# Kernel tuning notes

Hardware: AMD Instinct MI355X
Metric: run time of the kernel (lower is better)

Reference implementation:

```python
import jax, jax.numpy as jnp
import numpy as np

B, T = 192, 50
VOCAB = 24000
EMBED = 300
HID2 = 2000          # 2*HIDDEN_SIZE
MAXOUT = 300         # DIMEN_MAXOUT_UNIT
QV = 300             # DIMEN_QUALITY_VECTOR
H2 = 100             # LSTM hidden


def setup_inputs():
    key = jax.random.key(0)
    ks = jax.random.split(key, 24)
    s = 0.02
    inp = {
        'dec_out': jax.random.normal(ks[0], (B, T, HID2), jnp.float32),
        'y': jax.random.randint(ks[1], (B, T), 0, VOCAB, jnp.int64 if jax.config.jax_enable_x64 else jnp.int32),
        'contex': jax.random.normal(ks[2], (B, T, HID2), jnp.float32),
        'embed_table': jax.random.normal(ks[3], (VOCAB, EMBED), jnp.float32) * s,
        'W1': jax.random.uniform(ks[4], (VOCAB, QV), jnp.float32),  # torch.rand
        'S_w': jax.random.normal(ks[5], (2 * MAXOUT, HID2), jnp.float32) * s,
        'S_b': jnp.zeros((2 * MAXOUT,), jnp.float32),
        'V_w': jax.random.normal(ks[6], (2 * MAXOUT, 2 * EMBED), jnp.float32) * s,
        'V_b': jnp.zeros((2 * MAXOUT,), jnp.float32),
        'C0_w': jax.random.normal(ks[7], (2 * MAXOUT, HID2), jnp.float32) * s,
        'C0_b': jnp.zeros((2 * MAXOUT,), jnp.float32),
        'W2_w': jax.random.normal(ks[8], (QV, MAXOUT), jnp.float32) * s,
        'W2_b': jnp.zeros((QV,), jnp.float32),
        'wih0': jax.random.normal(ks[9], (4 * H2, QV), jnp.float32) * s,
        'whh0': jax.random.normal(ks[10], (4 * H2, H2), jnp.float32) * s,
        'bih0': jnp.zeros((4 * H2,), jnp.float32),
        'bhh0': jnp.zeros((4 * H2,), jnp.float32),
        'wih1': jax.random.normal(ks[11], (4 * H2, H2), jnp.float32) * s,
        'whh1': jax.random.normal(ks[12], (4 * H2, H2), jnp.float32) * s,
        'bih1': jnp.zeros((4 * H2,), jnp.float32),
        'bhh1': jnp.zeros((4 * H2,), jnp.float32),
        'Wqe_w': jax.random.normal(ks[13], (1, H2), jnp.float32) * s,
        'Wqe_b': jnp.zeros((1,), jnp.float32),
    }
    return inp


def _lstm_layer(x, Wih, Whh, bih, bhh):
    # x: [B, T, D] -> outputs [B, T, H]; torch gate order i, f, g, o
    Bb = x.shape[0]
    H = Whh.shape[1]
    xT = jnp.swapaxes(x, 0, 1)  # [T, B, D]

    def step(carry, xt):
        h, c = carry
        g = xt @ Wih.T + h @ Whh.T + bih + bhh
        i, f, gg, o = jnp.split(g, 4, axis=-1)
        i = jax.nn.sigmoid(i); f = jax.nn.sigmoid(f)
        gg = jnp.tanh(gg); o = jax.nn.sigmoid(o)
        c = f * c + i * gg
        h = o * jnp.tanh(c)
        return (h, c), h

    h0 = jnp.zeros((Bb, H), x.dtype)
    (_, _), hs = jax.lax.scan(step, (h0, h0), xT)
    return jnp.swapaxes(hs, 0, 1)


def reference(dec_out, y, contex, embed_table, W1, S_w, S_b, V_w, V_b,
              C0_w, C0_b, W2_w, W2_b, wih0, whh0, bih0, bhh0,
              wih1, whh1, bih1, bhh1, Wqe_w, Wqe_b):
    Bb, Tt, _ = dec_out.shape
    embed = embed_table[y]  # [B, T, EMBED]
    idx = jnp.arange(Tt)
    li = jnp.where(idx == 0, 1, idx - 1)          # left neighbor (i==0 -> 1)
    ri = jnp.where(idx == Tt - 1, Tt - 2, idx + 1)  # right neighbor (i==T-1 -> T-2)
    tensor2 = jnp.concatenate([embed[:, li], embed[:, ri]], axis=-1)  # [B,T,600]
    t_long = (dec_out @ S_w.T + S_b) + (tensor2 @ V_w.T + V_b) + (contex @ C0_w.T + C0_b)
    # maxout over consecutive pairs: t[...,i] = max(t_long[...,2i], t_long[...,2i+1])
    t = t_long.reshape(Bb, Tt, MAXOUT, 2).max(axis=-1)
    a = t @ W2_w.T + W2_b                        # [B,T,QV]
    logits = a @ W1.T                            # [B,T,VOCAB]
    b = jax.nn.log_softmax(logits.reshape(Bb * Tt, -1), axis=1)
    quality = W1[y] * a                          # [B,T,QV]
    mask = (y == 0)
    index1 = jnp.where(mask.any(axis=1), mask.argmax(axis=1), Tt - 1)
    h = _lstm_layer(quality, wih0, whh0, bih0, bhh0)
    h = _lstm_layer(h, wih1, whh1, bih1, bhh1)   # [B,T,H2]
    s_sel = h[jnp.arange(Bb), index1]            # [B,H2]
    QE_score = jax.nn.sigmoid(s_sel @ Wqe_w.T + Wqe_b)  # [B,1]
    return (b, QE_score)
```

## Files before the change

kernel.cpp:

```cpp
#include <hip/hip_runtime.h>

typedef unsigned short u16;
typedef __attribute__((ext_vector_type(4))) float f32x4;
typedef __attribute__((ext_vector_type(8))) short bf16x8;
typedef __attribute__((ext_vector_type(4))) unsigned short u16x4;
typedef __attribute__((ext_vector_type(8))) unsigned short u16x8;

#define BT 9600
#define VOCAB 24000
#define NCB 188

__device__ __forceinline__ u16 f2b(float f){
  union { float f; unsigned u; } c; c.f = f;
  unsigned u = c.u;
  return (u16)((u + 0x7FFFu + ((u >> 16) & 1u)) >> 16);
}
__device__ __forceinline__ float b2f(u16 v){
  union { unsigned u; float f; } c; c.u = ((unsigned)v) << 16;
  return c.f;
}

#define GLD16(g, l) __builtin_amdgcn_global_load_lds( \
    (__attribute__((address_space(1))) void*)(g), \
    (__attribute__((address_space(3))) void*)(l), 16, 0, 0)

__device__ __forceinline__ void gemm_core(
    const u16* __restrict__ A, const u16* __restrict__ B,
    int K, int brow, int bcol, u16* As, u16* Bs, f32x4 acc[4][4])
{
  const int tid  = threadIdx.x;
  const int w    = tid >> 6;
  const int lane = tid & 63;
  const int wm = w >> 1, wn = w & 1;

  const f32x4 fz = {0.f, 0.f, 0.f, 0.f};
  #pragma unroll
  for (int m = 0; m < 4; ++m)
    #pragma unroll
    for (int n = 0; n < 4; ++n) acc[m][n] = fz;

  const int nkt = K >> 6;

  auto stage = [&](int kt, int buf) {
    #pragma unroll
    for (int i = 0; i < 4; ++i) {
      int gl  = i * 256 + tid;
      int row = gl >> 3;
      int g   = (gl & 7) ^ (row & 7);
      const u16* ga = A + (size_t)(brow + row) * K + (kt << 6) + (g << 3);
      GLD16(ga, As + buf * 8192 + (size_t)(i * 256 + w * 64) * 8);
      const u16* gb = B + (size_t)(bcol + row) * K + (kt << 6) + (g << 3);
      GLD16(gb, Bs + buf * 8192 + (size_t)(i * 256 + w * 64) * 8);
    }
  };

  stage(0, 0);
  int cur = 0;
  for (int kt = 0; kt < nkt; ++kt) {
    if (kt + 1 < nkt) {
      stage(kt + 1, cur ^ 1);
      asm volatile("s_waitcnt vmcnt(8)" ::: "memory");
    } else {
      asm volatile("s_waitcnt vmcnt(0)" ::: "memory");
    }
    __builtin_amdgcn_s_barrier();
    asm volatile("" ::: "memory");
    const u16* Ab = As + cur * 8192;
    const u16* Bb = Bs + cur * 8192;
    #pragma unroll
    for (int kk = 0; kk < 2; ++kk) {
      bf16x8 af[4], bf[4];
      #pragma unroll
      for (int m = 0; m < 4; ++m) {
        int row = wm * 64 + m * 16 + (lane & 15);
        int g   = (kk * 4 + (lane >> 4)) ^ (row & 7);
        af[m] = *(const bf16x8*)(Ab + row * 64 + g * 8);
      }
      #pragma unroll
      for (int n = 0; n < 4; ++n) {
        int row = wn * 64 + n * 16 + (lane & 15);
        int g   = (kk * 4 + (lane >> 4)) ^ (row & 7);
        bf[n] = *(const bf16x8*)(Bb + row * 64 + g * 8);
      }
      #pragma unroll
      for (int m = 0; m < 4; ++m)
        #pragma unroll
        for (int n = 0; n < 4; ++n)
          acc[m][n] = __builtin_amdgcn_mfma_f32_16x16x32_bf16(af[m], bf[n], acc[m][n], 0, 0, 0);
    }
    asm volatile("" ::: "memory");
    __builtin_amdgcn_s_barrier();
    cur ^= 1;
  }
}

__device__ __forceinline__ void prep_main_body(
    const float* __restrict__ dec, const float* __restrict__ ctx,
    u16* __restrict__ Xcat, int tid)
{
  if (tid >= 9600 * 500) return;
  int r = tid / 500, k8 = (tid % 500) * 8;
  const float* src = (k8 < 2000) ? dec + (size_t)r * 2000 + k8
                                 : ctx + (size_t)r * 2000 + (k8 - 2000);
  const float4* s4 = (const float4*)src;
  float4 v0 = s4[0], v1 = s4[1];
  u16x8 o;
  o[0] = f2b(v0.x); o[1] = f2b(v0.y); o[2] = f2b(v0.z); o[3] = f2b(v0.w);
  o[4] = f2b(v1.x); o[5] = f2b(v1.y); o[6] = f2b(v1.z); o[7] = f2b(v1.w);
  *(u16x8*)(Xcat + (size_t)r * 4608 + k8) = o;
}

__device__ __forceinline__ void prep_emb_body(
    const int* __restrict__ y, const float* __restrict__ etab,
    u16* __restrict__ Xcat, int tid)
{
  if (tid >= 9600 * 152) return;
  int r = tid / 152, u = tid % 152;
  u16* xr = Xcat + (size_t)r * 4608;
  if (u >= 150) {
    int base = (u == 150) ? 4300 : 4604;
    u16x4 z; z[0] = 0; z[1] = 0; z[2] = 0; z[3] = 0;
    *(u16x4*)(xr + base) = z;
    return;
  }
  int t = r % 50;
  int side = u / 75, j4 = (u % 75) * 4;
  int tt = (side == 0) ? (t == 0 ? 1 : t - 1) : (t == 49 ? 48 : t + 1);
  int tok = y[r - t + tt];
  float4 v = *(const float4*)(etab + (size_t)tok * 300 + j4);
  u16x4 o; o[0] = f2b(v.x); o[1] = f2b(v.y); o[2] = f2b(v.z); o[3] = f2b(v.w);
  *(u16x4*)(xr + (side == 0 ? 4000 : 4304) + j4) = o;
}

__device__ __forceinline__ void wcat_body(
    const float* __restrict__ Sw, const float* __restrict__ C0w, const float* __restrict__ Vw,
    const float* __restrict__ Sb, const float* __restrict__ Vb, const float* __restrict__ C0b,
    u16* __restrict__ Wcat, float* __restrict__ biasc, int tid)
{
  if (tid >= 640 * 4608) return;
  int n = tid / 4608, k = tid % 4608;
  float v = 0.f;
  if (n < 600) {
    if (k < 2000)                  v = Sw[n * 2000 + k];
    else if (k < 4000)             v = C0w[n * 2000 + (k - 2000)];
    else if (k < 4300)             v = Vw[n * 600 + (k - 4000)];
    else if (k >= 4304 && k < 4604) v = Vw[n * 600 + 300 + (k - 4304)];
  }
  Wcat[tid] = f2b(v);
  if (k == 0) biasc[n] = (n < 600) ? (Sb[n] + Vb[n] + C0b[n]) : 0.f;
}

__device__ __forceinline__ void conv_body(
    const float* __restrict__ src, u16* __restrict__ dst,
    int srows, int scols, int drows, int dcols4, int tid)
{
  if (tid >= drows * dcols4) return;
  int r = tid / dcols4, c4 = (tid % dcols4) * 4;
  u16x4 o; o[0] = 0; o[1] = 0; o[2] = 0; o[3] = 0;
  if (r < srows && c4 < scols) {
    float4 v = *(const float4*)(src + (size_t)r * scols + c4);
    o[0] = f2b(v.x); o[1] = f2b(v.y); o[2] = f2b(v.z); o[3] = f2b(v.w);
  }
  *(u16x4*)(dst + (size_t)r * (dcols4 * 4) + c4) = o;
}

__global__ __launch_bounds__(256) void k_prep_all(
    const float* __restrict__ dec, const float* __restrict__ ctx,
    const int* __restrict__ y, const float* __restrict__ etab,
    const float* __restrict__ Sw, const float* __restrict__ C0w,
    const float* __restrict__ Vw, const float* __restrict__ Sb,
    const float* __restrict__ Vb, const float* __restrict__ C0b,
    const float* __restrict__ W1, const float* __restrict__ W2w,
    const float* __restrict__ wih0, const float* __restrict__ wih1,
    u16* __restrict__ Xcat, u16* __restrict__ Wcat, float* __restrict__ biasc,
    u16* __restrict__ W1b, u16* __restrict__ W2b,
    u16* __restrict__ wih0b, u16* __restrict__ wih1b)
{
  int bid = blockIdx.x, th = threadIdx.x;
  if (bid < 18750)      prep_main_body(dec, ctx, Xcat, bid * 256 + th);
  else if (bid < 24450) prep_emb_body(y, etab, Xcat, (bid - 18750) * 256 + th);
  else if (bid < 35970) wcat_body(Sw, C0w, Vw, Sb, Vb, C0b, Wcat, biasc, (bid - 24450) * 256 + th);
  else if (bid < 43490) conv_body(W1,   W1b,   24000, 300, 24064, 80, (bid - 35970) * 256 + th);
  else if (bid < 43610) conv_body(W2w,  W2b,   300,   300, 384,   80, (bid - 43490) * 256 + th);
  else if (bid < 43770) conv_body(wih0, wih0b, 400,   300, 512,   80, (bid - 43610) * 256 + th);
  else                  conv_body(wih1, wih1b, 400,   100, 512,   32, (bid - 43770) * 256 + th);
}

__global__ __launch_bounds__(256) void k_gemm_tlong(
    const u16* __restrict__ Xcat, const u16* __restrict__ Wcat,
    const float* __restrict__ biasc, u16* __restrict__ tb)
{
  __shared__ u16 As[16384], Bs[16384];
  f32x4 acc[4][4];
  int brow = blockIdx.y * 128, bcol = blockIdx.x * 128;
  gemm_core(Xcat, Wcat, 4608, brow, bcol, As, Bs, acc);
  int lane = threadIdx.x & 63, w = threadIdx.x >> 6;
  int wm = w >> 1, wn = w & 1;
  #pragma unroll
  for (int m = 0; m < 4; ++m)
    #pragma unroll
    for (int n = 0; n < 4; ++n)
      #pragma unroll
      for (int r = 0; r < 4; ++r) {
        int row = brow + wm * 64 + m * 16 + ((lane >> 4) << 2) + r;
        int col = bcol + wn * 64 + n * 16 + (lane & 15);
        float v = acc[m][n][r] + biasc[col];
        float o = __shfl_xor(v, 1);
        float t = fmaxf(v, o);
        if ((lane & 1) == 0)
          tb[(size_t)row * 320 + (col >> 1)] = f2b(t);
      }
}

__global__ __launch_bounds__(256) void k_gemm_a(
    const u16* __restrict__ tb, const u16* __restrict__ W2b,
    const float* __restrict__ W2bias, const float* __restrict__ W1,
    const int* __restrict__ y, u16* __restrict__ ab, u16* __restrict__ qb)
{
  __shared__ u16 As[16384], Bs[16384];
  f32x4 acc[4][4];
  int brow = blockIdx.y * 128, bcol = blockIdx.x * 128;
  gemm_core(tb, W2b, 320, brow, bcol, As, Bs, acc);
  int lane = threadIdx.x & 63, w = threadIdx.x >> 6;
  int wm = w >> 1, wn = w & 1;
  #pragma unroll
  for (int m = 0; m < 4; ++m)
    #pragma unroll
    for (int n = 0; n < 4; ++n)
      #pragma unroll
      for (int r = 0; r < 4; ++r) {
        int row = brow + wm * 64 + m * 16 + ((lane >> 4) << 2) + r;
        int col = bcol + wn * 64 + n * 16 + (lane & 15);
        if (col < 320) {
          float bias = (col < 300) ? W2bias[col] : 0.f;
          float a = acc[m][n][r] + bias;
          ab[(size_t)row * 320 + col] = f2b(a);
          float q = 0.f;
          if (col < 300) {
            int yv = y[row];
            q = a * W1[(size_t)yv * 300 + col];
          }
          qb[(size_t)row * 320 + col] = f2b(q);
        }
      }
}

__global__ __launch_bounds__(256) void k_gemm_logits_bf16(
    const u16* __restrict__ ab, const u16* __restrict__ W1b,
    u16* __restrict__ lb, float* __restrict__ part, int rb0)
{
  __shared__ u16 smem[32768];
  __shared__ float rowsum[128][2];
  f32x4 acc[4][4];
  int brow = (rb0 + blockIdx.y) * 128, bcol = blockIdx.x * 128;
  gemm_core(ab, W1b, 320, brow, bcol, smem, smem + 16384, acc);
  int lane = threadIdx.x & 63, w = threadIdx.x >> 6;
  int wm = w >> 1, wn = w & 1;
  #pragma unroll
  for (int m = 0; m < 4; ++m)
    #pragma unroll
    for (int r = 0; r < 4; ++r) {
      int lrow = wm * 64 + m * 16 + ((lane >> 4) << 2) + r;
      float es = 0.f;
      #pragma unroll
      for (int n = 0; n < 4; ++n) {
        int lcol = wn * 64 + n * 16 + (lane & 15);
        float v = acc[m][n][r];
        smem[lrow * 136 + lcol] = f2b(v);
        if (bcol + lcol < VOCAB) es += __expf(v);
      }
      es += __shfl_xor(es, 1); es += __shfl_xor(es, 2);
      es += __shfl_xor(es, 4); es += __shfl_xor(es, 8);
      if ((lane & 15) == 0) rowsum[lrow][wn] = es;
    }
  __syncthreads();
  if (threadIdx.x < 128)
    part[(size_t)(brow + threadIdx.x) * NCB + blockIdx.x] =
        rowsum[threadIdx.x][0] + rowsum[threadIdx.x][1];
  int lrow_base = blockIdx.y * 128;
  #pragma unroll
  for (int j = 0; j < 8; ++j) {
    int ch   = j * 256 + threadIdx.x;
    int rowl = ch >> 4;
    int c16  = (ch & 15) << 3;
    u16x8 v = *(const u16x8*)(smem + rowl * 136 + c16);
    *(u16x8*)(lb + (size_t)(lrow_base + rowl) * 24064 + bcol + c16) = v;
  }
}

__global__ __launch_bounds__(256) void k_gemm_logits_f32(
    const u16* __restrict__ ab, const u16* __restrict__ W1b,
    float* __restrict__ dout, float* __restrict__ part)
{
  __shared__ u16 As[16384], Bs[16384];
  __shared__ float rowsum[128][2];
  f32x4 acc[4][4];
  int brow = blockIdx.y * 128, bcol = blockIdx.x * 128;
  gemm_core(ab, W1b, 320, brow, bcol, As, Bs, acc);
  int lane = threadIdx.x & 63, w = threadIdx.x >> 6;
  int wm = w >> 1, wn = w & 1;
  #pragma unroll
  for (int m = 0; m < 4; ++m)
    #pragma unroll
    for (int r = 0; r < 4; ++r) {
      int lrow = wm * 64 + m * 16 + ((lane >> 4) << 2) + r;
      size_t grow = (size_t)(brow + lrow);
      float es = 0.f;
      #pragma unroll
      for (int n = 0; n < 4; ++n) {
        int col = bcol + wn * 64 + n * 16 + (lane & 15);
        float v = acc[m][n][r];
        if (col < VOCAB) {
          dout[grow * VOCAB + col] = v;
          es += __expf(v);
        }
      }
      es += __shfl_xor(es, 1); es += __shfl_xor(es, 2);
      es += __shfl_xor(es, 4); es += __shfl_xor(es, 8);
      if ((lane & 15) == 0) rowsum[lrow][wn] = es;
    }
  __syncthreads();
  if (threadIdx.x < 128)
    part[(size_t)(brow + threadIdx.x) * NCB + blockIdx.x] =
        rowsum[threadIdx.x][0] + rowsum[threadIdx.x][1];
}

__global__ __launch_bounds__(256) void k_gemm_proj(
    const u16* __restrict__ Ab, const u16* __restrict__ Bb, int K,
    const float* __restrict__ b1, const float* __restrict__ b2, float* __restrict__ out)
{
  __shared__ u16 As[16384], Bs[16384];
  f32x4 acc[4][4];
  int brow = blockIdx.y * 128, bcol = blockIdx.x * 128;
  gemm_core(Ab, Bb, K, brow, bcol, As, Bs, acc);
  int lane = threadIdx.x & 63, w = threadIdx.x >> 6;
  int wm = w >> 1, wn = w & 1;
  #pragma unroll
  for (int m = 0; m < 4; ++m)
    #pragma unroll
    for (int n = 0; n < 4; ++n)
      #pragma unroll
      for (int r = 0; r < 4; ++r) {
        int row = brow + wm * 64 + m * 16 + ((lane >> 4) << 2) + r;
        int col = bcol + wn * 64 + n * 16 + (lane & 15);
        if (col < 400)
          out[(size_t)row * 400 + col] = acc[m][n][r] + b1[col] + b2[col];
      }
}

__global__ __launch_bounds__(256) void k_rowlog(
    const float* __restrict__ part, float* __restrict__ logl, int r0)
{
  int row = r0 + blockIdx.x * 4 + (threadIdx.x >> 6);
  int l = threadIdx.x & 63;
  const float* p = part + (size_t)row * NCB;
  float s = p[l] + p[l + 64] + (l < 60 ? p[l + 128] : 0.f);
  s += __shfl_xor(s, 1);  s += __shfl_xor(s, 2);  s += __shfl_xor(s, 4);
  s += __shfl_xor(s, 8);  s += __shfl_xor(s, 16); s += __shfl_xor(s, 32);
  if (l == 0) logl[row] = logf(s);
}

__global__ __launch_bounds__(256) void k_fixup(
    float4* __restrict__ out4, const float* __restrict__ logl)
{
  size_t i = (size_t)blockIdx.x * blockDim.x + threadIdx.x;
  size_t stride = (size_t)gridDim.x * blockDim.x;
  const size_t total = (size_t)BT * (VOCAB / 4);
  for (; i < total; i += stride) {
    size_t row = i / (VOCAB / 4);
    float l = logl[row];
    float4 v = out4[i];
    v.x -= l; v.y -= l; v.z -= l; v.w -= l;
    out4[i] = v;
  }
}

__global__ __launch_bounds__(256) void k_fixup_bf16(
    const u16* __restrict__ lb, const float* __restrict__ logl,
    float* __restrict__ out, int r0, int nrows)
{
  size_t i = (size_t)blockIdx.x * blockDim.x + threadIdx.x;
  size_t stride = (size_t)gridDim.x * blockDim.x;
  const size_t total = (size_t)nrows * (VOCAB / 8);
  for (; i < total; i += stride) {
    size_t rowl = i / (VOCAB / 8);
    int c8 = (int)(i % (VOCAB / 8)) * 8;
    size_t row = r0 + rowl;
    float l = logl[row];
    u16x8 v = *(const u16x8*)(lb + rowl * 24064 + c8);
    float4 o0, o1;
    o0.x = b2f(v[0]) - l; o0.y = b2f(v[1]) - l; o0.z = b2f(v[2]) - l; o0.w = b2f(v[3]) - l;
    o1.x = b2f(v[4]) - l; o1.y = b2f(v[5]) - l; o1.z = b2f(v[6]) - l; o1.w = b2f(v[7]) - l;
    float* op = out + row * VOCAB + c8;
    *(float4*)op = o0;
    *(float4*)(op + 4) = o1;
  }
}

__global__ __launch_bounds__(512) void k_lstm0(
    const float* __restrict__ xp0, const float* __restrict__ whh0, u16* __restrict__ h0b)
{
  int b = blockIdx.x, g = threadIdx.x;
  __shared__ float h[100];
  __shared__ float act[400];
  float wrow[100];
  if (g < 400) {
    const float4* wr = (const float4*)(whh0 + (size_t)g * 100);
    #pragma unroll
    for (int q = 0; q < 25; ++q) {
      float4 t = wr[q];
      wrow[4 * q] = t.x; wrow[4 * q + 1] = t.y; wrow[4 * q + 2] = t.z; wrow[4 * q + 3] = t.w;
    }
  }
  if (g < 100) h[g] = 0.f;
  float c = 0.f;
  __syncthreads();
  for (int t = 0; t < 50; ++t) {
    if (g < 400) {
      float s = xp0[(size_t)(b * 50 + t) * 400 + g];
      const float4* hv = (const float4*)h;
      #pragma unroll
      for (int q = 0; q < 25; ++q) {
        float4 hh = hv[q];
        s += wrow[4 * q] * hh.x + wrow[4 * q + 1] * hh.y
           + wrow[4 * q + 2] * hh.z + wrow[4 * q + 3] * hh.w;
      }
      act[g] = (g >= 200 && g < 300) ? tanhf(s) : 1.f / (1.f + __expf(-s));
    }
    __syncthreads();
    if (g < 100) {
      c = act[100 + g] * c + act[g] * act[200 + g];
      float hn = act[300 + g] * tanhf(c);
      h[g] = hn;
      h0b[(size_t)(b * 50 + t) * 128 + g] = f2b(hn);
    } else if (g < 128) {
      h0b[(size_t)(b * 50 + t) * 128 + g] = 0;
    }
    __syncthreads();
  }
}

__global__ __launch_bounds__(512) void k_lstm1(
    const float* __restrict__ xp1, const float* __restrict__ whh1,
    const int* __restrict__ y, const float* __restrict__ wqe,
    const float* __restrict__ wqeb, float* __restrict__ qout)
{
  int b = blockIdx.x, g = threadIdx.x;
  __shared__ float h[100];
  __shared__ float act[400];
  __shared__ float hsel[100];
  __shared__ int idx1;
  float wrow[100];
  if (g < 400) {
    const float4* wr = (const float4*)(whh1 + (size_t)g * 100);
    #pragma unroll
    for (int q = 0; q < 25; ++q) {
      float4 t = wr[q];
      wrow[4 * q] = t.x; wrow[4 * q + 1] = t.y; wrow[4 * q + 2] = t.z; wrow[4 * q + 3] = t.w;
    }
  }
  if (g == 0) {
    int ix = 49;
    for (int t = 0; t < 50; ++t) { if (y[b * 50 + t] == 0) { ix = t; break; } }
    idx1 = ix;
  }
  if (g < 100) { h[g] = 0.f; hsel[g] = 0.f; }
  float c = 0.f;
  __syncthreads();
  for (int t = 0; t < 50; ++t) {
    if (g < 400) {
      float s = xp1[(size_t)(b * 50 + t) * 400 + g];
      const float4* hv = (const float4*)h;
      #pragma unroll
      for (int q = 0; q < 25; ++q) {
        float4 hh = hv[q];
        s += wrow[4 * q] * hh.x + wrow[4 * q + 1] * hh.y
           + wrow[4 * q + 2] * hh.z + wrow[4 * q + 3] * hh.w;
      }
      act[g] = (g >= 200 && g < 300) ? tanhf(s) : 1.f / (1.f + __expf(-s));
    }
    __syncthreads();
    if (g < 100) {
      c = act[100 + g] * c + act[g] * act[200 + g];
      float hn = act[300 + g] * tanhf(c);
      h[g] = hn;
      if (t == idx1) hsel[g] = hn;
    }
    __syncthreads();
  }
  if (g == 0) {
    float s = wqeb[0];
    for (int j = 0; j < 100; ++j) s += hsel[j] * wqe[j];
    qout[b] = 1.f / (1.f + __expf(-s));
  }
}

extern "C" void kernel_launch(void* const* d_in, const int* in_sizes, int n_in,
                              void* d_out, int out_size, void* d_ws, size_t ws_size,
                              hipStream_t stream) {
  const float* dec  = (const float*)d_in[0];
  const int*   y    = (const int*)d_in[1];
  const float* ctx  = (const float*)d_in[2];
  const float* etab = (const float*)d_in[3];
  const float* W1   = (const float*)d_in[4];
  const float* Sw   = (const float*)d_in[5];
  const float* Sb   = (const float*)d_in[6];
  const float* Vw   = (const float*)d_in[7];
  const float* Vb   = (const float*)d_in[8];
  const float* C0w  = (const float*)d_in[9];
  const float* C0b  = (const float*)d_in[10];
  const float* W2w  = (const float*)d_in[11];
  const float* W2bias = (const float*)d_in[12];
  const float* wih0 = (const float*)d_in[13];
  const float* whh0 = (const float*)d_in[14];
  const float* bih0 = (const float*)d_in[15];
  const float* bhh0 = (const float*)d_in[16];
  const float* wih1 = (const float*)d_in[17];
  const float* whh1 = (const float*)d_in[18];
  const float* bih1 = (const float*)d_in[19];
  const float* bhh1 = (const float*)d_in[20];
  const float* wqe  = (const float*)d_in[21];
  const float* wqeb = (const float*)d_in[22];

  char* ws = (char*)d_ws;
  u16*   Xcat  = (u16*)(ws + 0);
  u16*   Wcat  = (u16*)(ws + 88473600);
  float* biasc = (float*)(ws + 94371840);
  u16*   tb    = (u16*)(ws + 94374400);
  u16*   W2b   = (u16*)(ws + 100518400);
  u16*   ab    = (u16*)(ws + 100764160);
  u16*   qb    = (u16*)(ws + 106908160);
  u16*   W1b   = (u16*)(ws + 113052160);
  float* part  = (float*)(ws + 128453120);
  float* logl  = (float*)(ws + 135672320);
  u16*   wih0b = (u16*)(ws + 135710720);
  float* xp0   = (float*)(ws + 136038400);
  u16*   h0b   = (u16*)(ws + 151398400);
  u16*   wih1b = (u16*)(ws + 153856000);
  float* xp1   = (float*)(ws + 153987072);
  u16*   lb    = (u16*)(ws + 169347072);
  const size_t WS_NEED_BF16 = 169347072ull + 154009600ull;
  const bool use_bf16_logits = (ws_size >= WS_NEED_BF16);

  float* bout  = (float*)d_out;
  float* qeout = bout + (size_t)BT * VOCAB;

  k_prep_all<<<43834, 256, 0, stream>>>(dec, ctx, y, etab, Sw, C0w, Vw, Sb, Vb, C0b,
                                        W1, W2w, wih0, wih1,
                                        Xcat, Wcat, biasc, W1b, W2b, wih0b, wih1b);

  k_gemm_tlong<<<dim3(5, 75), 256, 0, stream>>>(Xcat, Wcat, biasc, tb);
  k_gemm_a<<<dim3(3, 75), 256, 0, stream>>>(tb, W2b, W2bias, W1, y, ab, qb);

  if (use_bf16_logits) {
    for (int c = 0; c < 3; ++c) {
      k_gemm_logits_bf16<<<dim3(NCB, 25), 256, 0, stream>>>(ab, W1b, lb, part, 25 * c);
      k_rowlog<<<800, 256, 0, stream>>>(part, logl, 3200 * c);
      k_fixup_bf16<<<2048, 256, 0, stream>>>(lb, logl, bout, 3200 * c, 3200);
    }
  } else {
    k_gemm_logits_f32<<<dim3(NCB, 75), 256, 0, stream>>>(ab, W1b, bout, part);
    k_rowlog<<<2400, 256, 0, stream>>>(part, logl, 0);
    k_fixup<<<4096, 256, 0, stream>>>((float4*)bout, logl);
  }

  k_gemm_proj<<<dim3(4, 75), 256, 0, stream>>>(qb, wih0b, 320, bih0, bhh0, xp0);
  k_lstm0<<<192, 512, 0, stream>>>(xp0, whh0, h0b);
  k_gemm_proj<<<dim3(4, 75), 256, 0, stream>>>(h0b, wih1b, 128, bih1, bhh1, xp1);
  k_lstm1<<<192, 512, 0, stream>>>(xp1, whh1, y, wqe, wqeb, qeout);
}
```

Before: 1.048 ms.

## Fuse serial LSTM chain into logits/softmax stages via heterogeneous block launches

Replaces the three-chunk logits/rowlog/fixup loop and the separate LSTM kernels with four combined kernels. Each combined kernel assigns some blocks to the bandwidth-heavy logits, rowlog or fixup work and others to the latency-bound LSTM steps and projections, so the serial LSTM chain overlaps with them. It also remaps the t_long GEMM block indices so neighbouring row tiles land on the same XCD. The bf16 logits buffer now has to hold all 9600 rows, so the workspace requirement grows. If the workspace is too small, the code falls back to the f32 path and gets no overlap.

```diff
diff --git a/kernel.cpp b/kernel.cpp
--- a/kernel.cpp
+++ b/kernel.cpp
@@ -28,7 +28,7 @@
     const u16* __restrict__ A, const u16* __restrict__ B,
     int K, int brow, int bcol, u16* As, u16* Bs, f32x4 acc[4][4])
 {
-  const int tid  = threadIdx.x;
+  const int tid  = threadIdx.x & 255;
   const int w    = tid >> 6;
   const int lane = tid & 63;
   const int wm = w >> 1, wn = w & 1;
@@ -92,6 +92,27 @@
     __builtin_amdgcn_s_barrier();
     cur ^= 1;
   }
+}
+
+__device__ __forceinline__ void proj_epilogue(
+    f32x4 acc[4][4], int brow, int bcol,
+    const float* __restrict__ b1, const float* __restrict__ b2,
+    float* __restrict__ out)
+{
+  int tid = threadIdx.x & 255;
+  int lane = tid & 63, w = tid >> 6;
+  int wm = w >> 1, wn = w & 1;
+  #pragma unroll
+  for (int m = 0; m < 4; ++m)
+    #pragma unroll
+    for (int n = 0; n < 4; ++n)
+      #pragma unroll
+      for (int r = 0; r < 4; ++r) {
+        int row = brow + wm * 64 + m * 16 + ((lane >> 4) << 2) + r;
+        int col = bcol + wn * 64 + n * 16 + (lane & 15);
+        if (col < 400)
+          out[(size_t)row * 400 + col] = acc[m][n][r] + b1[col] + b2[col];
+      }
 }
 
 __device__ __forceinline__ void prep_main_body(
@@ -192,7 +213,12 @@
 {
   __shared__ u16 As[16384], Bs[16384];
   f32x4 acc[4][4];
-  int brow = blockIdx.y * 128, bcol = blockIdx.x * 128;
+  int L = blockIdx.x;
+  int xcd = L & 7, s = L >> 3;
+  int yy = (s / 5) * 8 + xcd;
+  int xx = s % 5;
+  if (yy >= 75) return;
+  int brow = yy * 128, bcol = xx * 128;
   gemm_core(Xcat, Wcat, 4608, brow, bcol, As, Bs, acc);
   int lane = threadIdx.x & 63, w = threadIdx.x >> 6;
   int wm = w >> 1, wn = w & 1;
@@ -245,14 +271,25 @@
       }
 }
 
-__global__ __launch_bounds__(256) void k_gemm_logits_bf16(
+__global__ __launch_bounds__(256) void k_s1(
     const u16* __restrict__ ab, const u16* __restrict__ W1b,
-    u16* __restrict__ lb, float* __restrict__ part, int rb0)
+    u16* __restrict__ lb, float* __restrict__ part,
+    const u16* __restrict__ qb, const u16* __restrict__ wih0b,
+    const float* __restrict__ bih0, const float* __restrict__ bhh0,
+    float* __restrict__ xp0)
 {
   __shared__ u16 smem[32768];
   __shared__ float rowsum[128][2];
   f32x4 acc[4][4];
-  int brow = (rb0 + blockIdx.y) * 128, bcol = blockIdx.x * 128;
+  int bid = blockIdx.x;
+  if (bid < 300) {
+    int brow = (bid / 4) * 128, bcol = (bid % 4) * 128;
+    gemm_core(qb, wih0b, 320, brow, bcol, smem, smem + 16384, acc);
+    proj_epilogue(acc, brow, bcol, bih0, bhh0, xp0);
+    return;
+  }
+  int g = bid - 300;
+  int brow = (g / NCB) * 128, bcol = (g % NCB) * 128;
   gemm_core(ab, W1b, 320, brow, bcol, smem, smem + 16384, acc);
   int lane = threadIdx.x & 63, w = threadIdx.x >> 6;
   int wm = w >> 1, wn = w & 1;
@@ -275,17 +312,191 @@
     }
   __syncthreads();
   if (threadIdx.x < 128)
-    part[(size_t)(brow + threadIdx.x) * NCB + blockIdx.x] =
+    part[(size_t)(brow + threadIdx.x) * NCB + (g % NCB)] =
         rowsum[threadIdx.x][0] + rowsum[threadIdx.x][1];
-  int lrow_base = blockIdx.y * 128;
   #pragma unroll
   for (int j = 0; j < 8; ++j) {
     int ch   = j * 256 + threadIdx.x;
     int rowl = ch >> 4;
     int c16  = (ch & 15) << 3;
     u16x8 v = *(const u16x8*)(smem + rowl * 136 + c16);
-    *(u16x8*)(lb + (size_t)(lrow_base + rowl) * 24064 + bcol + c16) = v;
-  }
+    *(u16x8*)(lb + (size_t)(brow + rowl) * 24064 + bcol + c16) = v;
+  }
+}
+
+__device__ __forceinline__ void lstm0_body(
+    const float* __restrict__ xp0, const float* __restrict__ whh0,
+    u16* __restrict__ h0b, int b)
+{
+  int g = threadIdx.x;
+  __shared__ float h[100];
+  __shared__ float act[400];
+  float wrow[100];
+  if (g < 400) {
+    const float4* wr = (const float4*)(whh0 + (size_t)g * 100);
+    #pragma unroll
+    for (int q = 0; q < 25; ++q) {
+      float4 t = wr[q];
+      wrow[4 * q] = t.x; wrow[4 * q + 1] = t.y; wrow[4 * q + 2] = t.z; wrow[4 * q + 3] = t.w;
+    }
+  }
+  if (g < 100) h[g] = 0.f;
+  float c = 0.f;
+  __syncthreads();
+  for (int t = 0; t < 50; ++t) {
+    if (g < 400) {
+      float s = xp0[(size_t)(b * 50 + t) * 400 + g];
+      const float4* hv = (const float4*)h;
+      #pragma unroll
+      for (int q = 0; q < 25; ++q) {
+        float4 hh = hv[q];
+        s += wrow[4 * q] * hh.x + wrow[4 * q + 1] * hh.y
+           + wrow[4 * q + 2] * hh.z + wrow[4 * q + 3] * hh.w;
+      }
+      act[g] = (g >= 200 && g < 300) ? tanhf(s) : 1.f / (1.f + __expf(-s));
+    }
+    __syncthreads();
+    if (g < 100) {
+      c = act[100 + g] * c + act[g] * act[200 + g];
+      float hn = act[300 + g] * tanhf(c);
+      h[g] = hn;
+      h0b[(size_t)(b * 50 + t) * 128 + g] = f2b(hn);
+    } else if (g < 128) {
+      h0b[(size_t)(b * 50 + t) * 128 + g] = 0;
+    }
+    __syncthreads();
+  }
+}
+
+__device__ __forceinline__ void lstm1_body(
+    const float* __restrict__ xp1, const float* __restrict__ whh1,
+    const int* __restrict__ y, const float* __restrict__ wqe,
+    const float* __restrict__ wqeb, float* __restrict__ qout, int b)
+{
+  int g = threadIdx.x;
+  __shared__ float h[100];
+  __shared__ float act[400];
+  __shared__ float hsel[100];
+  __shared__ int idx1;
+  float wrow[100];
+  if (g < 400) {
+    const float4* wr = (const float4*)(whh1 + (size_t)g * 100);
+    #pragma unroll
+    for (int q = 0; q < 25; ++q) {
+      float4 t = wr[q];
+      wrow[4 * q] = t.x; wrow[4 * q + 1] = t.y; wrow[4 * q + 2] = t.z; wrow[4 * q + 3] = t.w;
+    }
+  }
+  if (g == 0) {
+    int ix = 49;
+    for (int t = 0; t < 50; ++t) { if (y[b * 50 + t] == 0) { ix = t; break; } }
+    idx1 = ix;
+  }
+  if (g < 100) { h[g] = 0.f; hsel[g] = 0.f; }
+  float c = 0.f;
+  __syncthreads();
+  for (int t = 0; t < 50; ++t) {
+    if (g < 400) {
+      float s = xp1[(size_t)(b * 50 + t) * 400 + g];
+      const float4* hv = (const float4*)h;
+      #pragma unroll
+      for (int q = 0; q < 25; ++q) {
+        float4 hh = hv[q];
+        s += wrow[4 * q] * hh.x + wrow[4 * q + 1] * hh.y
+           + wrow[4 * q + 2] * hh.z + wrow[4 * q + 3] * hh.w;
+      }
+      act[g] = (g >= 200 && g < 300) ? tanhf(s) : 1.f / (1.f + __expf(-s));
+    }
+    __syncthreads();
+    if (g < 100) {
+      c = act[100 + g] * c + act[g] * act[200 + g];
+      float hn = act[300 + g] * tanhf(c);
+      h[g] = hn;
+      if (t == idx1) hsel[g] = hn;
+    }
+    __syncthreads();
+  }
+  if (g == 0) {
+    float s = wqeb[0];
+    for (int j = 0; j < 100; ++j) s += hsel[j] * wqe[j];
+    qout[b] = 1.f / (1.f + __expf(-s));
+  }
+}
+
+__device__ __forceinline__ void fixup_body(
+    const u16* __restrict__ lb, const float* __restrict__ logl,
+    float* __restrict__ out, int r0, int nrows, int bid, int nb, int nthreads)
+{
+  size_t i = (size_t)bid * nthreads + threadIdx.x;
+  size_t stride = (size_t)nb * nthreads;
+  const size_t total = (size_t)nrows * (VOCAB / 8);
+  for (; i < total; i += stride) {
+    size_t rowl = i / (VOCAB / 8);
+    int c8 = (int)(i % (VOCAB / 8)) * 8;
+    size_t row = r0 + rowl;
+    float l = logl[row];
+    u16x8 v = *(const u16x8*)(lb + row * 24064 + c8);
+    float4 o0, o1;
+    o0.x = b2f(v[0]) - l; o0.y = b2f(v[1]) - l; o0.z = b2f(v[2]) - l; o0.w = b2f(v[3]) - l;
+    o1.x = b2f(v[4]) - l; o1.y = b2f(v[5]) - l; o1.z = b2f(v[6]) - l; o1.w = b2f(v[7]) - l;
+    float* op = out + row * VOCAB + c8;
+    *(float4*)op = o0;
+    *(float4*)(op + 4) = o1;
+  }
+}
+
+__global__ __launch_bounds__(512) void k_s2(
+    const float* __restrict__ part, float* __restrict__ logl,
+    const float* __restrict__ xp0, const float* __restrict__ whh0,
+    u16* __restrict__ h0b)
+{
+  int bid = blockIdx.x;
+  if (bid < 1200) {
+    int row = bid * 8 + (threadIdx.x >> 6);
+    int l = threadIdx.x & 63;
+    const float* p = part + (size_t)row * NCB;
+    float s = p[l] + p[l + 64] + (l < 60 ? p[l + 128] : 0.f);
+    s += __shfl_xor(s, 1);  s += __shfl_xor(s, 2);  s += __shfl_xor(s, 4);
+    s += __shfl_xor(s, 8);  s += __shfl_xor(s, 16); s += __shfl_xor(s, 32);
+    if (l == 0) logl[row] = logf(s);
+    return;
+  }
+  lstm0_body(xp0, whh0, h0b, bid - 1200);
+}
+
+__global__ __launch_bounds__(256) void k_s3(
+    const u16* __restrict__ lb, const float* __restrict__ logl,
+    float* __restrict__ out,
+    const u16* __restrict__ h0b, const u16* __restrict__ wih1b,
+    const float* __restrict__ bih1, const float* __restrict__ bhh1,
+    float* __restrict__ xp1)
+{
+  int bid = blockIdx.x;
+  if (bid < 3072) {
+    fixup_body(lb, logl, out, 0, 6400, bid, 3072, 256);
+    return;
+  }
+  __shared__ u16 As[16384], Bs[16384];
+  f32x4 acc[4][4];
+  int pb = bid - 3072;
+  int brow = (pb / 4) * 128, bcol = (pb % 4) * 128;
+  gemm_core(h0b, wih1b, 128, brow, bcol, As, Bs, acc);
+  proj_epilogue(acc, brow, bcol, bih1, bhh1, xp1);
+}
+
+__global__ __launch_bounds__(512) void k_s4(
+    const u16* __restrict__ lb, const float* __restrict__ logl,
+    float* __restrict__ out,
+    const float* __restrict__ xp1, const float* __restrict__ whh1,
+    const int* __restrict__ y, const float* __restrict__ wqe,
+    const float* __restrict__ wqeb, float* __restrict__ qout)
+{
+  int bid = blockIdx.x;
+  if (bid < 192) {
+    lstm1_body(xp1, whh1, y, wqe, wqeb, qout, bid);
+    return;
+  }
+  fixup_body(lb, logl, out, 6400, 3200, bid - 192, 1024, 512);
 }
 
 __global__ __launch_bounds__(256) void k_gemm_logits_f32(
@@ -310,10 +521,7 @@
       for (int n = 0; n < 4; ++n) {
         int col = bcol + wn * 64 + n * 16 + (lane & 15);
         float v = acc[m][n][r];
-        if (col < VOCAB) {
-          dout[grow * VOCAB + col] = v;
-          es += __expf(v);
-        }
+        if (col < VOCAB) { dout[grow * VOCAB + col] = v; es += __expf(v); }
       }
       es += __shfl_xor(es, 1); es += __shfl_xor(es, 2);
       es += __shfl_xor(es, 4); es += __shfl_xor(es, 8);
@@ -333,25 +541,13 @@
   f32x4 acc[4][4];
   int brow = blockIdx.y * 128, bcol = blockIdx.x * 128;
   gemm_core(Ab, Bb, K, brow, bcol, As, Bs, acc);
-  int lane = threadIdx.x & 63, w = threadIdx.x >> 6;
-  int wm = w >> 1, wn = w & 1;
-  #pragma unroll
-  for (int m = 0; m < 4; ++m)
-    #pragma unroll
-    for (int n = 0; n < 4; ++n)
-      #pragma unroll
-      for (int r = 0; r < 4; ++r) {
-        int row = brow + wm * 64 + m * 16 + ((lane >> 4) << 2) + r;
-        int col = bcol + wn * 64 + n * 16 + (lane & 15);
-        if (col < 400)
-          out[(size_t)row * 400 + col] = acc[m][n][r] + b1[col] + b2[col];
-      }
-}
-
-__global__ __launch_bounds__(256) void k_rowlog(
-    const float* __restrict__ part, float* __restrict__ logl, int r0)
-{
-  int row = r0 + blockIdx.x * 4 + (threadIdx.x >> 6);
+  proj_epilogue(acc, brow, bcol, b1, b2, out);
+}
+
+__global__ __launch_bounds__(256) void k_rowlog256(
+    const float* __restrict__ part, float* __restrict__ logl)
+{
+  int row = blockIdx.x * 4 + (threadIdx.x >> 6);
   int l = threadIdx.x & 63;
   const float* p = part + (size_t)row * NCB;
   float s = p[l] + p[l + 64] + (l < 60 ? p[l + 128] : 0.f);
@@ -360,7 +556,7 @@
   if (l == 0) logl[row] = logf(s);
 }
 
-__global__ __launch_bounds__(256) void k_fixup(
+__global__ __launch_bounds__(256) void k_fixup_f32(
     float4* __restrict__ out4, const float* __restrict__ logl)
 {
   size_t i = (size_t)blockIdx.x * blockDim.x + threadIdx.x;
@@ -375,125 +571,15 @@
   }
 }
 
-__global__ __launch_bounds__(256) void k_fixup_bf16(
-    const u16* __restrict__ lb, const float* __restrict__ logl,
-    float* __restrict__ out, int r0, int nrows)
-{
-  size_t i = (size_t)blockIdx.x * blockDim.x + threadIdx.x;
-  size_t stride = (size_t)gridDim.x * blockDim.x;
-  const size_t total = (size_t)nrows * (VOCAB / 8);
-  for (; i < total; i += stride) {
-    size_t rowl = i / (VOCAB / 8);
-    int c8 = (int)(i % (VOCAB / 8)) * 8;
-    size_t row = r0 + rowl;
-    float l = logl[row];
-    u16x8 v = *(const u16x8*)(lb + rowl * 24064 + c8);
-    float4 o0, o1;
-    o0.x = b2f(v[0]) - l; o0.y = b2f(v[1]) - l; o0.z = b2f(v[2]) - l; o0.w = b2f(v[3]) - l;
-    o1.x = b2f(v[4]) - l; o1.y = b2f(v[5]) - l; o1.z = b2f(v[6]) - l; o1.w = b2f(v[7]) - l;
-    float* op = out + row * VOCAB + c8;
-    *(float4*)op = o0;
-    *(float4*)(op + 4) = o1;
-  }
-}
-
 __global__ __launch_bounds__(512) void k_lstm0(
     const float* __restrict__ xp0, const float* __restrict__ whh0, u16* __restrict__ h0b)
-{
-  int b = blockIdx.x, g = threadIdx.x;
-  __shared__ float h[100];
-  __shared__ float act[400];
-  float wrow[100];
-  if (g < 400) {
-    const float4* wr = (const float4*)(whh0 + (size_t)g * 100);
-    #pragma unroll
-    for (int q = 0; q < 25; ++q) {
-      float4 t = wr[q];
-      wrow[4 * q] = t.x; wrow[4 * q + 1] = t.y; wrow[4 * q + 2] = t.z; wrow[4 * q + 3] = t.w;
-    }
-  }
-  if (g < 100) h[g] = 0.f;
-  float c = 0.f;
-  __syncthreads();
-  for (int t = 0; t < 50; ++t) {
-    if (g < 400) {
-      float s = xp0[(size_t)(b * 50 + t) * 400 + g];
-      const float4* hv = (const float4*)h;
-      #pragma unroll
-      for (int q = 0; q < 25; ++q) {
-        float4 hh = hv[q];
-        s += wrow[4 * q] * hh.x + wrow[4 * q + 1] * hh.y
-           + wrow[4 * q + 2] * hh.z + wrow[4 * q + 3] * hh.w;
-      }
-      act[g] = (g >= 200 && g < 300) ? tanhf(s) : 1.f / (1.f + __expf(-s));
-    }
-    __syncthreads();
-    if (g < 100) {
-      c = act[100 + g] * c + act[g] * act[200 + g];
-      float hn = act[300 + g] * tanhf(c);
-      h[g] = hn;
-      h0b[(size_t)(b * 50 + t) * 128 + g] = f2b(hn);
-    } else if (g < 128) {
-      h0b[(size_t)(b * 50 + t) * 128 + g] = 0;
-    }
-    __syncthreads();
-  }
-}
+{ lstm0_body(xp0, whh0, h0b, blockIdx.x); }
 
 __global__ __launch_bounds__(512) void k_lstm1(
     const float* __restrict__ xp1, const float* __restrict__ whh1,
     const int* __restrict__ y, const float* __restrict__ wqe,
     const float* __restrict__ wqeb, float* __restrict__ qout)
-{
-  int b = blockIdx.x, g = threadIdx.x;
-  __shared__ float h[100];
-  __shared__ float act[400];
-  __shared__ float hsel[100];
-  __shared__ int idx1;
-  float wrow[100];
-  if (g < 400) {
-    const float4* wr = (const float4*)(whh1 + (size_t)g * 100);
-    #pragma unroll
-    for (int q = 0; q < 25; ++q) {
-      float4 t = wr[q];
-      wrow[4 * q] = t.x; wrow[4 * q + 1] = t.y; wrow[4 * q + 2] = t.z; wrow[4 * q + 3] = t.w;
-    }
-  }
-  if (g == 0) {
-    int ix = 49;
-    for (int t = 0; t < 50; ++t) { if (y[b * 50 + t] == 0) { ix = t; break; } }
-    idx1 = ix;
-  }
-  if (g < 100) { h[g] = 0.f; hsel[g] = 0.f; }
-  float c = 0.f;
-  __syncthreads();
-  for (int t = 0; t < 50; ++t) {
-    if (g < 400) {
-      float s = xp1[(size_t)(b * 50 + t) * 400 + g];
-      const float4* hv = (const float4*)h;
-      #pragma unroll
-      for (int q = 0; q < 25; ++q) {
-        float4 hh = hv[q];
-        s += wrow[4 * q] * hh.x + wrow[4 * q + 1] * hh.y
-           + wrow[4 * q + 2] * hh.z + wrow[4 * q + 3] * hh.w;
-      }
-      act[g] = (g >= 200 && g < 300) ? tanhf(s) : 1.f / (1.f + __expf(-s));
-    }
-    __syncthreads();
-    if (g < 100) {
-      c = act[100 + g] * c + act[g] * act[200 + g];
-      float hn = act[300 + g] * tanhf(c);
-      h[g] = hn;
-      if (t == idx1) hsel[g] = hn;
-    }
-    __syncthreads();
-  }
-  if (g == 0) {
-    float s = wqeb[0];
-    for (int j = 0; j < 100; ++j) s += hsel[j] * wqe[j];
-    qout[b] = 1.f / (1.f + __expf(-s));
-  }
-}
+{ lstm1_body(xp1, whh1, y, wqe, wqeb, qout, blockIdx.x); }
 
 extern "C" void kernel_launch(void* const* d_in, const int* in_sizes, int n_in,
                               void* d_out, int out_size, void* d_ws, size_t ws_size,
@@ -539,7 +625,7 @@
   u16*   wih1b = (u16*)(ws + 153856000);
   float* xp1   = (float*)(ws + 153987072);
   u16*   lb    = (u16*)(ws + 169347072);
-  const size_t WS_NEED_BF16 = 169347072ull + 154009600ull;
+  const size_t WS_NEED_BF16 = 169347072ull + 462028800ull;
   const bool use_bf16_logits = (ws_size >= WS_NEED_BF16);
 
   float* bout  = (float*)d_out;
@@ -549,23 +635,21 @@
                                         W1, W2w, wih0, wih1,
                                         Xcat, Wcat, biasc, W1b, W2b, wih0b, wih1b);
 
-  k_gemm_tlong<<<dim3(5, 75), 256, 0, stream>>>(Xcat, Wcat, biasc, tb);
+  k_gemm_tlong<<<400, 256, 0, stream>>>(Xcat, Wcat, biasc, tb);
   k_gemm_a<<<dim3(3, 75), 256, 0, stream>>>(tb, W2b, W2bias, W1, y, ab, qb);
 
   if (use_bf16_logits) {
-    for (int c = 0; c < 3; ++c) {
-      k_gemm_logits_bf16<<<dim3(NCB, 25), 256, 0, stream>>>(ab, W1b, lb, part, 25 * c);
-      k_rowlog<<<800, 256, 0, stream>>>(part, logl, 3200 * c);
-      k_fixup_bf16<<<2048, 256, 0, stream>>>(lb, logl, bout, 3200 * c, 3200);
-    }
+    k_s1<<<14400, 256, 0, stream>>>(ab, W1b, lb, part, qb, wih0b, bih0, bhh0, xp0);
+    k_s2<<<1392, 512, 0, stream>>>(part, logl, xp0, whh0, h0b);
+    k_s3<<<3372, 256, 0, stream>>>(lb, logl, bout, h0b, wih1b, bih1, bhh1, xp1);
+    k_s4<<<1216, 512, 0, stream>>>(lb, logl, bout, xp1, whh1, y, wqe, wqeb, qeout);
   } else {
     k_gemm_logits_f32<<<dim3(NCB, 75), 256, 0, stream>>>(ab, W1b, bout, part);
-    k_rowlog<<<2400, 256, 0, stream>>>(part, logl, 0);
-    k_fixup<<<4096, 256, 0, stream>>>((float4*)bout, logl);
-  }
-
-  k_gemm_proj<<<dim3(4, 75), 256, 0, stream>>>(qb, wih0b, 320, bih0, bhh0, xp0);
-  k_lstm0<<<192, 512, 0, stream>>>(xp0, whh0, h0b);
-  k_gemm_proj<<<dim3(4, 75), 256, 0, stream>>>(h0b, wih1b, 128, bih1, bhh1, xp1);
-  k_lstm1<<<192, 512, 0, stream>>>(xp1, whh1, y, wqe, wqeb, qeout);
-}
+    k_rowlog256<<<2400, 256, 0, stream>>>(part, logl);
+    k_fixup_f32<<<4096, 256, 0, stream>>>((float4*)bout, logl);
+    k_gemm_proj<<<dim3(4, 75), 256, 0, stream>>>(qb, wih0b, 320, bih0, bhh0, xp0);
+    k_lstm0<<<192, 512, 0, stream>>>(xp0, whh0, h0b);
+    k_gemm_proj<<<dim3(4, 75), 256, 0, stream>>>(h0b, wih1b, 128, bih1, bhh1, xp1);
+    k_lstm1<<<192, 512, 0, stream>>>(xp1, whh1, y, wqe, wqeb, qeout);
+  }
+}
```

New measurement: 943.6 us. 1.11x faster.
